# Kernel optimization log

Hardware: AMD Instinct MI355X
Metric: run time of the kernel (lower is better)

The kernel has to match this reference:

```python
import jax, jax.numpy as jnp
import numpy as np
from jax.scipy.special import logsumexp

B, T, S, V = 64, 1024, 512, 1024


def setup_inputs() -> dict:
    key = jax.random.key(0)
    k_obs, k_emis, k_trans, k_prior = jax.random.split(key, 4)
    observations = jax.random.randint(k_obs, (B, T), 0, V, dtype=jnp.int32)
    emission_table = jax.random.normal(k_emis, (V, S), dtype=jnp.float32)
    transitions = jax.random.normal(k_trans, (S, S), dtype=jnp.float32)
    prior = jax.random.normal(k_prior, (S,), dtype=jnp.float32)
    return {
        "observations": observations,
        "emission_table": emission_table,
        "transitions": transitions,
        "prior": prior,
    }


def reference(observations, emission_table, transitions, prior):
    # alpha_0[b, s] = emission_logits(obs_0)[b, s] + prior[s]
    alpha0 = emission_table[observations[:, 0]] + prior  # [B, S]

    def step(alpha, obs_t):
        # new_alpha[b, j] = emis[b, j] + logsumexp_i(alpha[b, i] + trans[i, j])
        e = emission_table[obs_t]  # [B, S]
        a = e + logsumexp(alpha[:, :, None] + transitions[None, :, :], axis=1)
        return a, None

    # scan over time steps 1..T-1; xs is [T-1, B]
    alpha, _ = jax.lax.scan(step, alpha0, observations[:, 1:].T)
    return logsumexp(alpha, axis=1)  # [B]
```

## Files before the change

kernel.cpp:

```cpp
#include <hip/hip_runtime.h>


constexpr int Bn = 64, Tn = 1024, Sn = 512;
#define L2E 1.44269504f

typedef int v4i __attribute__((ext_vector_type(4)));

#if __has_builtin(__builtin_amdgcn_update_dpp)
template <int CTRL>
__device__ __forceinline__ float dpp_fmax(float x) {
    int s = __builtin_bit_cast(int, x);
    int d = __builtin_amdgcn_update_dpp(s, s, CTRL, 0xf, 0xf, false);
    return fmaxf(x, __builtin_bit_cast(float, d));
}
__device__ __forceinline__ float wave_max64(float x) {
    x = dpp_fmax<0x121>(x);
    x = dpp_fmax<0x122>(x);
    x = dpp_fmax<0x124>(x);
    x = dpp_fmax<0x128>(x);
    x = dpp_fmax<0x142>(x);
    x = dpp_fmax<0x143>(x);
    return __builtin_bit_cast(float,
        __builtin_amdgcn_readlane(__builtin_bit_cast(int, x), 63));
}
__device__ __forceinline__ float max_of_8_pattern(float x) {
    x = dpp_fmax<0x121>(x);
    x = dpp_fmax<0x122>(x);
    x = dpp_fmax<0x124>(x);
    return x;
}
#else
__device__ __forceinline__ float wave_max64(float x) {
    #pragma unroll
    for (int off = 32; off; off >>= 1) x = fmaxf(x, __shfl_xor(x, off, 64));
    return x;
}
__device__ __forceinline__ float max_of_8_pattern(float x) {
    #pragma unroll
    for (int off = 1; off < 8; off <<= 1) x = fmaxf(x, __shfl_xor(x, off, 64));
    return x;
}
#endif

__device__ __forceinline__ int bfrag_addr(int i, int c) {
    return ((((c >> 4) * 8 + (i >> 6)) * 64) + ((i >> 4) & 3) * 16 + (c & 15)) * 16
           + (i & 15);
}

__global__ __launch_bounds__(256) void prep_rows(
    const float* __restrict__ trans, unsigned char* __restrict__ EqB,
    float* __restrict__ rowmax)
{
    const int i = blockIdx.x;
    const int j = threadIdx.x;
    const int lane = j & 63, wv = j >> 6;
    float t0 = trans[i * Sn + j];
    float t1 = trans[i * Sn + j + 256];
    float m = fmaxf(t0, t1);
    #pragma unroll
    for (int off = 32; off; off >>= 1) m = fmaxf(m, __shfl_xor(m, off, 64));
    __shared__ float rm[4];
    if (lane == 0) rm[wv] = m;
    __syncthreads();
    m = fmaxf(fmaxf(rm[0], rm[1]), fmaxf(rm[2], rm[3]));
    if (j == 0) rowmax[i] = m;
    int q0 = __float2int_rn(127.f * __expf(t0 - m));
    int q1 = __float2int_rn(127.f * __expf(t1 - m));
    EqB[bfrag_addr(i, j)] = (unsigned char)q0;
    EqB[bfrag_addr(i, j + 256)] = (unsigned char)q1;
}

__global__ __launch_bounds__(512) void prep_scale(
    const float* __restrict__ rowmax, float* __restrict__ lr,
    float* __restrict__ Cp)
{
    const int i = threadIdx.x;
    const int lane = i & 63, wv = i >> 6;
    float m = rowmax[i];
    float rm = m;
    #pragma unroll
    for (int off = 32; off; off >>= 1) rm = fmaxf(rm, __shfl_xor(rm, off, 64));
    __shared__ float red[8];
    if (lane == 0) red[wv] = rm;
    __syncthreads();
    float RM = red[0];
    #pragma unroll
    for (int w = 1; w < 8; ++w) RM = fmaxf(RM, red[w]);
    lr[i] = (m - RM) * L2E + 6.98868469f;
    if (i == 0) *Cp = RM - 9.68837417f;
}

__global__ __launch_bounds__(512, 2) void hmm_fwd(
    const int* __restrict__ obs,
    const float* __restrict__ emis,
    const float* __restrict__ prior,
    const v4i* __restrict__ EqB4,
    const float* __restrict__ lr,
    const float* __restrict__ Cp,
    float* __restrict__ out)
{
    const int b = blockIdx.x;
    const int tid = threadIdx.x;
    const int lane = tid & 63, wv = tid >> 6;
    const int q = lane >> 4;

    __shared__ int obs_s[Tn];
    __shared__ __align__(16) unsigned char Pq[2][Sn];
    __shared__ float redm[2][8];
    __shared__ float reds[8];

    obs_s[tid] = obs[b * Tn + tid];
    obs_s[tid + 512] = obs[b * Tn + 512 + tid];

    v4i Bf[4][8];
    #pragma unroll
    for (int tau = 0; tau < 4; ++tau)
        #pragma unroll
        for (int kap = 0; kap < 8; ++kap)
            Bf[tau][kap] = EqB4[((wv * 4 + tau) * 8 + kap) * 64 + lane];

    const float lr_t = lr[tid];
    const float C = *Cp;

    __syncthreads();

    float a = emis[obs_s[0] * Sn + tid] + prior[tid];
    float e_next = emis[obs_s[1] * Sn + tid];

    for (int t = 1; t < Tn; ++t) {
        const int pb = t & 1;

        float mw = wave_max64(a);
        if (lane == 0) redm[pb][wv] = mw;
        __syncthreads();
        float m = max_of_8_pattern(redm[pb][lane & 7]);

        int gi = __float2int_rn(exp2f(fmaf(a - m, L2E, lr_t)));
        Pq[pb][tid] = (unsigned char)gi;
        __syncthreads();

        float e_cur = e_next;
        if (t < Tn - 1) e_next = emis[obs_s[t + 1] * Sn + tid];

        const unsigned char* Pbase = Pq[pb] + q * 16;
        v4i Af[8];
        #pragma unroll
        for (int kap = 0; kap < 8; ++kap)
            Af[kap] = *(const v4i*)(Pbase + kap * 64);

        v4i acc[4];
        #pragma unroll
        for (int tau = 0; tau < 4; ++tau) {
            v4i z = {0, 0, 0, 0};
            #pragma unroll
            for (int kap = 0; kap < 8; ++kap)
                z = __builtin_amdgcn_mfma_i32_16x16x64_i8(Af[kap], Bf[tau][kap],
                                                          z, 0, 0, 0);
            acc[tau] = z;
        }

        int idot = (lane < 16) ? acc[0].x
                 : (lane < 32) ? acc[1].x
                 : (lane < 48) ? acc[2].x
                               : acc[3].x;

        a = e_cur + m + C + __logf((float)idot);
    }

    float m = a;
    #pragma unroll
    for (int off = 32; off; off >>= 1) m = fmaxf(m, __shfl_xor(m, off, 64));
    if (lane == 0) redm[0][wv] = m;
    __syncthreads();
    #pragma unroll
    for (int w = 0; w < 8; ++w) m = fmaxf(m, redm[0][w]);

    float s = __expf(a - m);
    #pragma unroll
    for (int off = 32; off; off >>= 1) s += __shfl_xor(s, off, 64);
    if (lane == 0) reds[wv] = s;
    __syncthreads();
    if (tid == 0) {
        float tot = 0.f;
        #pragma unroll
        for (int w = 0; w < 8; ++w) tot += reds[w];
        out[b] = m + __logf(tot);
    }
}

extern "C" void kernel_launch(void* const* d_in, const int* in_sizes, int n_in,
                              void* d_out, int out_size, void* d_ws, size_t ws_size,
                              hipStream_t stream) {
    const int*   obs   = (const int*)d_in[0];
    const float* emis  = (const float*)d_in[1];
    const float* trans = (const float*)d_in[2];
    const float* prior = (const float*)d_in[3];
    float* out = (float*)d_out;

    unsigned char* EqB = (unsigned char*)d_ws;
    float* rowmax = (float*)(EqB + Sn * Sn);
    float* lr     = rowmax + Sn;
    float* Cp     = lr + Sn;

    prep_rows<<<Sn, 256, 0, stream>>>(trans, EqB, rowmax);
    prep_scale<<<1, Sn, 0, stream>>>(rowmax, lr, Cp);
    hmm_fwd<<<Bn, Sn, 0, stream>>>(obs, emis, prior,
                                   (const v4i*)EqB, lr, Cp, out);
}
```

Before: 1.010 ms.

## Use per-wave max for quantization to drop one barrier per step

Each wave now quantizes its alpha slice against its own wave-local max, so the block-wide max barrier before writing Pq is removed and only one __syncthreads per time step remains. To compensate, the int8 MFMA reduction is split per K-chunk (per wave). The integer partial sums are then rescaled in float by exp(wave_max - global_max) and combined. This adds eight separate MFMA accumulations per tau instead of chained ones, plus readlane broadcasts and FMAs. It also changes the quantization precision per wave.

```diff
diff --git a/kernel.cpp b/kernel.cpp
--- a/kernel.cpp
+++ b/kernel.cpp
@@ -29,6 +29,10 @@
     x = dpp_fmax<0x124>(x);
     return x;
 }
+__device__ __forceinline__ float lane_bcast(float x, int l) {
+    return __builtin_bit_cast(float,
+        __builtin_amdgcn_readlane(__builtin_bit_cast(int, x), l));
+}
 #else
 __device__ __forceinline__ float wave_max64(float x) {
     #pragma unroll
@@ -39,6 +43,9 @@
     #pragma unroll
     for (int off = 1; off < 8; off <<= 1) x = fmaxf(x, __shfl_xor(x, off, 64));
     return x;
+}
+__device__ __forceinline__ float lane_bcast(float x, int l) {
+    return __shfl(x, l, 64);
 }
 #endif
 
@@ -132,13 +139,14 @@
 
         float mw = wave_max64(a);
         if (lane == 0) redm[pb][wv] = mw;
-        __syncthreads();
-        float m = max_of_8_pattern(redm[pb][lane & 7]);
-
-        int gi = __float2int_rn(exp2f(fmaf(a - m, L2E, lr_t)));
+        int gi = __float2int_rn(exp2f(fmaf(a - mw, L2E, lr_t)));
         Pq[pb][tid] = (unsigned char)gi;
         __syncthreads();
 
+        float r = redm[pb][lane & 7];
+        float m = max_of_8_pattern(r);
+        float sv = exp2f((r - m) * L2E);
+
         float e_cur = e_next;
         if (t < Tn - 1) e_next = emis[obs_s[t + 1] * Sn + tid];
 
@@ -148,23 +156,25 @@
         for (int kap = 0; kap < 8; ++kap)
             Af[kap] = *(const v4i*)(Pbase + kap * 64);
 
-        v4i acc[4];
+        int xw[8];
         #pragma unroll
         for (int tau = 0; tau < 4; ++tau) {
-            v4i z = {0, 0, 0, 0};
+            const v4i z = {0, 0, 0, 0};
             #pragma unroll
-            for (int kap = 0; kap < 8; ++kap)
-                z = __builtin_amdgcn_mfma_i32_16x16x64_i8(Af[kap], Bf[tau][kap],
-                                                          z, 0, 0, 0);
-            acc[tau] = z;
+            for (int w = 0; w < 8; ++w) {
+                v4i acc = __builtin_amdgcn_mfma_i32_16x16x64_i8(
+                    Af[w], Bf[tau][w], z, 0, 0, 0);
+                if (tau == 0) xw[w] = acc.x;
+                else         xw[w] = (q == tau) ? acc.x : xw[w];
+            }
         }
 
-        int idot = (lane < 16) ? acc[0].x
-                 : (lane < 32) ? acc[1].x
-                 : (lane < 48) ? acc[2].x
-                               : acc[3].x;
-
-        a = e_cur + m + C + __logf((float)idot);
+        float fs = 0.f;
+        #pragma unroll
+        for (int w = 0; w < 8; ++w)
+            fs = fmaf(lane_bcast(sv, w), (float)xw[w], fs);
+
+        a = e_cur + m + C + __logf(fs);
     }
 
     float m = a;
```

New measurement: 1.086 ms. 7.5% more time.

## Split transition matvec between MFMA and VALU sdot4 paths

Applied to the files above, without the earlier changes.

Halves the K dimension handled by the int8 MFMA chain. The other half of the 512-state contraction (states 256..511) is now computed on vector ALUs using sdot4 against a register-resident repacked transition slice, 64 ints per thread. The aim is to shorten the serial MFMA dependency chain on each time step by overlapping matrix-core and VALU work. The cost is much higher register pressure (64 extra VGPRs), which may hurt the 2-blocks occupancy target or cause spills, plus an extra packed copy of the transitions in workspace.

```diff
diff --git a/kernel.cpp b/kernel.cpp
--- a/kernel.cpp
+++ b/kernel.cpp
@@ -5,6 +5,18 @@
 #define L2E 1.44269504f
 
 typedef int v4i __attribute__((ext_vector_type(4)));
+
+__device__ __forceinline__ int dot4(int e, int p, int acc) {
+#if __has_builtin(__builtin_amdgcn_sdot4)
+    return __builtin_amdgcn_sdot4(e, p, acc, false);
+#else
+    acc += (int)(signed char)(e) * (int)(signed char)(p);
+    acc += (int)(signed char)(e >> 8) * (int)(signed char)(p >> 8);
+    acc += (int)(signed char)(e >> 16) * (int)(signed char)(p >> 16);
+    acc += (int)(signed char)(e >> 24) * (int)(signed char)(p >> 24);
+    return acc;
+#endif
+}
 
 #if __has_builtin(__builtin_amdgcn_update_dpp)
 template <int CTRL>
@@ -49,7 +61,7 @@
 
 __global__ __launch_bounds__(256) void prep_rows(
     const float* __restrict__ trans, unsigned char* __restrict__ EqB,
-    float* __restrict__ rowmax)
+    unsigned char* __restrict__ E2, float* __restrict__ rowmax)
 {
     const int i = blockIdx.x;
     const int j = threadIdx.x;
@@ -68,6 +80,8 @@
     int q1 = __float2int_rn(127.f * __expf(t1 - m));
     EqB[bfrag_addr(i, j)] = (unsigned char)q0;
     EqB[bfrag_addr(i, j + 256)] = (unsigned char)q1;
+    E2[(i >> 2) * 2048 + j * 4 + (i & 3)] = (unsigned char)q0;
+    E2[(i >> 2) * 2048 + (j + 256) * 4 + (i & 3)] = (unsigned char)q1;
 }
 
 __global__ __launch_bounds__(512) void prep_scale(
@@ -95,6 +109,7 @@
     const float* __restrict__ emis,
     const float* __restrict__ prior,
     const v4i* __restrict__ EqB4,
+    const int* __restrict__ E2u,
     const float* __restrict__ lr,
     const float* __restrict__ Cp,
     float* __restrict__ out)
@@ -112,12 +127,16 @@
     obs_s[tid] = obs[b * Tn + tid];
     obs_s[tid + 512] = obs[b * Tn + 512 + tid];
 
-    v4i Bf[4][8];
+    v4i Bf[4][4];
     #pragma unroll
     for (int tau = 0; tau < 4; ++tau)
         #pragma unroll
-        for (int kap = 0; kap < 8; ++kap)
+        for (int kap = 0; kap < 4; ++kap)
             Bf[tau][kap] = EqB4[((wv * 4 + tau) * 8 + kap) * 64 + lane];
+
+    int Ed[64];
+    #pragma unroll
+    for (int k = 0; k < 64; ++k) Ed[k] = E2u[(64 + k) * Sn + tid];
 
     const float lr_t = lr[tid];
     const float C = *Cp;
@@ -143,9 +162,9 @@
         if (t < Tn - 1) e_next = emis[obs_s[t + 1] * Sn + tid];
 
         const unsigned char* Pbase = Pq[pb] + q * 16;
-        v4i Af[8];
-        #pragma unroll
-        for (int kap = 0; kap < 8; ++kap)
+        v4i Af[4];
+        #pragma unroll
+        for (int kap = 0; kap < 4; ++kap)
             Af[kap] = *(const v4i*)(Pbase + kap * 64);
 
         v4i acc[4];
@@ -153,18 +172,30 @@
         for (int tau = 0; tau < 4; ++tau) {
             v4i z = {0, 0, 0, 0};
             #pragma unroll
-            for (int kap = 0; kap < 8; ++kap)
+            for (int kap = 0; kap < 4; ++kap)
                 z = __builtin_amdgcn_mfma_i32_16x16x64_i8(Af[kap], Bf[tau][kap],
                                                           z, 0, 0, 0);
             acc[tau] = z;
         }
 
-        int idot = (lane < 16) ? acc[0].x
-                 : (lane < 32) ? acc[1].x
-                 : (lane < 48) ? acc[2].x
-                               : acc[3].x;
-
-        a = e_cur + m + C + __logf((float)idot);
+        const v4i* Pd = (const v4i*)(Pq[pb] + 256);
+        int ac0 = 0, ac1 = 0, ac2 = 0, ac3 = 0;
+        #pragma unroll
+        for (int c = 0; c < 16; ++c) {
+            v4i p = Pd[c];
+            ac0 = dot4(Ed[4 * c + 0], p.x, ac0);
+            ac1 = dot4(Ed[4 * c + 1], p.y, ac1);
+            ac2 = dot4(Ed[4 * c + 2], p.z, ac2);
+            ac3 = dot4(Ed[4 * c + 3], p.w, ac3);
+        }
+        int idsum = (ac0 + ac1) + (ac2 + ac3);
+
+        int im = (lane < 16) ? acc[0].x
+               : (lane < 32) ? acc[1].x
+               : (lane < 48) ? acc[2].x
+                             : acc[3].x;
+
+        a = e_cur + m + C + __logf((float)(im + idsum));
     }
 
     float m = a;
@@ -198,12 +229,14 @@
     float* out = (float*)d_out;
 
     unsigned char* EqB = (unsigned char*)d_ws;
-    float* rowmax = (float*)(EqB + Sn * Sn);
+    unsigned char* E2  = EqB + Sn * Sn;
+    float* rowmax = (float*)(E2 + Sn * Sn);
     float* lr     = rowmax + Sn;
     float* Cp     = lr + Sn;
 
-    prep_rows<<<Sn, 256, 0, stream>>>(trans, EqB, rowmax);
+    prep_rows<<<Sn, 256, 0, stream>>>(trans, EqB, E2, rowmax);
     prep_scale<<<1, Sn, 0, stream>>>(rowmax, lr, Cp);
     hmm_fwd<<<Bn, Sn, 0, stream>>>(obs, emis, prior,
-                                   (const v4i*)EqB, lr, Cp, out);
-}
+                                   (const v4i*)EqB, (const int*)E2,
+                                   lr, Cp, out);
+}
```

After: 1.182 ms. 17.0% more time.

## Switch forward recursion matmul to block-scaled FP6 MFMA with per-block exponents

Applied to the files above, without the earlier changes.

Replaces the int8 16x16x64 MFMA path with the gfx950 scaled f8f6f4 16x16x128 MFMA, using FP6 (e2m3) operands and per-32-element E8M0 block scales for both the transition matrix and the per-step probability vector. Halves the MFMA instruction count per step and shrinks the shared-memory probability buffer. It adds in-register 6-bit packing through DPP and shuffles each step, plus readlane scale broadcasts. It also merges the two prep kernels into one. The trade is lower mantissa precision against better dynamic range, and the per-step packing adds latency to a sequential chain.

```diff
diff --git a/kernel.cpp b/kernel.cpp
--- a/kernel.cpp
+++ b/kernel.cpp
@@ -4,13 +4,17 @@
 constexpr int Bn = 64, Tn = 1024, Sn = 512;
 #define L2E 1.44269504f
 
-typedef int v4i __attribute__((ext_vector_type(4)));
-
-#if __has_builtin(__builtin_amdgcn_update_dpp)
+typedef int v8i __attribute__((ext_vector_type(8)));
+typedef float v4f __attribute__((ext_vector_type(4)));
+
+template <int CTRL>
+__device__ __forceinline__ int dpp_i(int x) {
+    return __builtin_amdgcn_update_dpp(x, x, CTRL, 0xf, 0xf, false);
+}
 template <int CTRL>
 __device__ __forceinline__ float dpp_fmax(float x) {
     int s = __builtin_bit_cast(int, x);
-    int d = __builtin_amdgcn_update_dpp(s, s, CTRL, 0xf, 0xf, false);
+    int d = dpp_i<CTRL>(s);
     return fmaxf(x, __builtin_bit_cast(float, d));
 }
 __device__ __forceinline__ float wave_max64(float x) {
@@ -29,98 +33,91 @@
     x = dpp_fmax<0x124>(x);
     return x;
 }
-#else
-__device__ __forceinline__ float wave_max64(float x) {
-    #pragma unroll
-    for (int off = 32; off; off >>= 1) x = fmaxf(x, __shfl_xor(x, off, 64));
-    return x;
-}
-__device__ __forceinline__ float max_of_8_pattern(float x) {
-    #pragma unroll
-    for (int off = 1; off < 8; off <<= 1) x = fmaxf(x, __shfl_xor(x, off, 64));
-    return x;
-}
-#endif
-
-__device__ __forceinline__ int bfrag_addr(int i, int c) {
-    return ((((c >> 4) * 8 + (i >> 6)) * 64) + ((i >> 4) & 3) * 16 + (c & 15)) * 16
-           + (i & 15);
-}
-
-__global__ __launch_bounds__(256) void prep_rows(
-    const float* __restrict__ trans, unsigned char* __restrict__ EqB,
-    float* __restrict__ rowmax)
+__device__ __forceinline__ int rl_i(int x, int l) {
+    return __builtin_amdgcn_readlane(x, l);
+}
+
+__device__ __forceinline__ int e2m3_rn(float v) {
+    v = fminf(v, 7.5f);
+    float mult = v < 2.f ? 8.f : (v < 4.f ? 4.f : 2.f);
+    int   add  = v < 2.f ? 0   : (v < 4.f ? 8   : 16);
+    return (int)rintf(v * mult) + add;
+}
+
+__global__ __launch_bounds__(64) void prep_E6(
+    const float* __restrict__ trans, unsigned int* __restrict__ EqB6,
+    unsigned char* __restrict__ SBtab)
 {
-    const int i = blockIdx.x;
-    const int j = threadIdx.x;
-    const int lane = j & 63, wv = j >> 6;
-    float t0 = trans[i * Sn + j];
-    float t1 = trans[i * Sn + j + 256];
-    float m = fmaxf(t0, t1);
-    #pragma unroll
-    for (int off = 32; off; off >>= 1) m = fmaxf(m, __shfl_xor(m, off, 64));
-    __shared__ float rm[4];
-    if (lane == 0) rm[wv] = m;
-    __syncthreads();
-    m = fmaxf(fmaxf(rm[0], rm[1]), fmaxf(rm[2], rm[3]));
-    if (j == 0) rowmax[i] = m;
-    int q0 = __float2int_rn(127.f * __expf(t0 - m));
-    int q1 = __float2int_rn(127.f * __expf(t1 - m));
-    EqB[bfrag_addr(i, j)] = (unsigned char)q0;
-    EqB[bfrag_addr(i, j + 256)] = (unsigned char)q1;
-}
-
-__global__ __launch_bounds__(512) void prep_scale(
-    const float* __restrict__ rowmax, float* __restrict__ lr,
-    float* __restrict__ Cp)
-{
-    const int i = threadIdx.x;
-    const int lane = i & 63, wv = i >> 6;
-    float m = rowmax[i];
-    float rm = m;
-    #pragma unroll
-    for (int off = 32; off; off >>= 1) rm = fmaxf(rm, __shfl_xor(rm, off, 64));
-    __shared__ float red[8];
-    if (lane == 0) red[wv] = rm;
-    __syncthreads();
-    float RM = red[0];
-    #pragma unroll
-    for (int w = 1; w < 8; ++w) RM = fmaxf(RM, red[w]);
-    lr[i] = (m - RM) * L2E + 6.98868469f;
-    if (i == 0) *Cp = RM - 9.68837417f;
+    const int t = threadIdx.x;
+    const int j = blockIdx.x * 4 + (t >> 4);
+    const int rb = t & 15;
+
+    float tv[32]; float tmax = -1e30f;
+    #pragma unroll
+    for (int k = 0; k < 32; ++k) {
+        tv[k] = trans[(rb * 32 + k) * Sn + j];
+        tmax = fmaxf(tmax, tv[k]);
+    }
+    float e = ceilf(fmaf(tmax, L2E, -2.9068906f));
+
+    unsigned dw[6] = {0, 0, 0, 0, 0, 0};
+    #pragma unroll
+    for (int k = 0; k < 32; ++k) {
+        float v = exp2f(fmaf(tv[k], L2E, -e));
+        unsigned c = (unsigned)e2m3_rn(v);
+        int bit = 6 * k;
+        dw[bit >> 5] |= c << (bit & 31);
+        if ((bit & 31) > 26) dw[(bit >> 5) + 1] |= c >> (32 - (bit & 31));
+    }
+
+    int f = ((j >> 6) * 4 + ((j >> 4) & 3)) * 4 + (rb >> 2);
+    int lane = (rb & 3) * 16 + (j & 15);
+    unsigned base = (unsigned)(f * 64 + lane) * 6;
+    #pragma unroll
+    for (int d = 0; d < 6; ++d) EqB6[base + d] = dw[d];
+
+    int sb = 127 + (int)e;
+    SBtab[j * 16 + rb] = (unsigned char)(sb < 1 ? 1 : (sb > 254 ? 254 : sb));
 }
 
 __global__ __launch_bounds__(512, 2) void hmm_fwd(
     const int* __restrict__ obs,
     const float* __restrict__ emis,
     const float* __restrict__ prior,
-    const v4i* __restrict__ EqB4,
-    const float* __restrict__ lr,
-    const float* __restrict__ Cp,
+    const unsigned int* __restrict__ EqB6,
+    const unsigned char* __restrict__ SBtab,
     float* __restrict__ out)
 {
     const int b = blockIdx.x;
     const int tid = threadIdx.x;
     const int lane = tid & 63, wv = tid >> 6;
     const int q = lane >> 4;
+    const int hb = lane >> 5;
 
     __shared__ int obs_s[Tn];
-    __shared__ __align__(16) unsigned char Pq[2][Sn];
+    __shared__ __align__(16) unsigned int Pq6[2][96];
     __shared__ float redm[2][8];
     __shared__ float reds[8];
 
     obs_s[tid] = obs[b * Tn + tid];
     obs_s[tid + 512] = obs[b * Tn + 512 + tid];
 
-    v4i Bf[4][8];
-    #pragma unroll
-    for (int tau = 0; tau < 4; ++tau)
-        #pragma unroll
-        for (int kap = 0; kap < 8; ++kap)
-            Bf[tau][kap] = EqB4[((wv * 4 + tau) * 8 + kap) * 64 + lane];
-
-    const float lr_t = lr[tid];
-    const float C = *Cp;
+    v8i Bf8[4][4];
+    int SBv[4][4];
+    #pragma unroll
+    for (int tau = 0; tau < 4; ++tau) {
+        int col = wv * 64 + tau * 16 + (lane & 15);
+        #pragma unroll
+        for (int kap = 0; kap < 4; ++kap) {
+            const uint2* p = (const uint2*)(EqB6 +
+                (unsigned)((((wv * 4 + tau) * 4 + kap) * 64 + lane) * 6));
+            uint2 x0 = p[0], x1 = p[1], x2 = p[2];
+            v8i bb = {(int)x0.x, (int)x0.y, (int)x1.x, (int)x1.y,
+                      (int)x2.x, (int)x2.y, 0, 0};
+            Bf8[tau][kap] = bb;
+            SBv[tau][kap] = (int)SBtab[col * 16 + kap * 4 + q] * 0x01010101;
+        }
+    }
 
     __syncthreads();
 
@@ -133,38 +130,77 @@
         float mw = wave_max64(a);
         if (lane == 0) redm[pb][wv] = mw;
         __syncthreads();
-        float m = max_of_8_pattern(redm[pb][lane & 7]);
-
-        int gi = __float2int_rn(exp2f(fmaf(a - m, L2E, lr_t)));
-        Pq[pb][tid] = (unsigned char)gi;
+
+        float r = redm[pb][lane & 7];
+        float mAll = max_of_8_pattern(r);
+
+        float nf = fmaxf(floorf((r - mAll) * L2E), -110.f);
+        int sb = 126 + (int)nf;
+        int sbdup = sb * 0x01010101;
+
+        float nown = fmaxf(floorf((mw - mAll) * L2E), -110.f);
+
+        float v = exp2f(fmaf(a - mAll, L2E, 1.0f - nown));
+        int code = e2m3_rn(v);
+
+        int p1 = dpp_i<0xB1>(code);
+        int m1 = (lane & 1) ? (p1 | (code << 6)) : (code | (p1 << 6));
+        int p2 = dpp_i<0x4E>(m1);
+        int w24 = (lane & 2) ? (p2 | (m1 << 12)) : (m1 | (p2 << 12));
+
+        int rowbase = lane & 48;
+        int w1 = __shfl(w24, rowbase + 4, 64);
+        int w2 = __shfl(w24, rowbase + 8, 64);
+        int w3 = __shfl(w24, rowbase + 12, 64);
+        int sel = lane & 15;
+        unsigned dwv = sel == 0 ? (unsigned)(w24 | (w1 << 24))
+                     : sel == 1 ? (unsigned)(((unsigned)w1 >> 8) | (w2 << 16))
+                                : (unsigned)(((unsigned)w2 >> 16) | (w3 << 8));
+        if (sel < 3) Pq6[pb][3 * (tid >> 4) + sel] = dwv;
+
+        int ee0 = rl_i(sbdup, 0), ee1 = rl_i(sbdup, 1);
+        int ee2 = rl_i(sbdup, 2), ee3 = rl_i(sbdup, 3);
+        int ee4 = rl_i(sbdup, 4), ee5 = rl_i(sbdup, 5);
+        int ee6 = rl_i(sbdup, 6), ee7 = rl_i(sbdup, 7);
+        int sA0 = hb ? ee1 : ee0;
+        int sA1 = hb ? ee3 : ee2;
+        int sA2 = hb ? ee5 : ee4;
+        int sA3 = hb ? ee7 : ee6;
         __syncthreads();
 
         float e_cur = e_next;
         if (t < Tn - 1) e_next = emis[obs_s[t + 1] * Sn + tid];
 
-        const unsigned char* Pbase = Pq[pb] + q * 16;
-        v4i Af[8];
-        #pragma unroll
-        for (int kap = 0; kap < 8; ++kap)
-            Af[kap] = *(const v4i*)(Pbase + kap * 64);
-
-        v4i acc[4];
+        v8i Af8[4];
+        #pragma unroll
+        for (int kap = 0; kap < 4; ++kap) {
+            const uint2* pp = (const uint2*)(Pq6[pb] + kap * 24 + q * 6);
+            uint2 x0 = pp[0], x1 = pp[1], x2 = pp[2];
+            v8i aa = {(int)x0.x, (int)x0.y, (int)x1.x, (int)x1.y,
+                      (int)x2.x, (int)x2.y, 0, 0};
+            Af8[kap] = aa;
+        }
+
+        float accx[4];
         #pragma unroll
         for (int tau = 0; tau < 4; ++tau) {
-            v4i z = {0, 0, 0, 0};
+            v4f z = {0.f, 0.f, 0.f, 0.f};
             #pragma unroll
-            for (int kap = 0; kap < 8; ++kap)
-                z = __builtin_amdgcn_mfma_i32_16x16x64_i8(Af[kap], Bf[tau][kap],
-                                                          z, 0, 0, 0);
-            acc[tau] = z;
+            for (int kap = 0; kap < 4; ++kap) {
+                int sA = (kap == 0) ? sA0 : (kap == 1) ? sA1
+                         : (kap == 2) ? sA2 : sA3;
+                z = __builtin_amdgcn_mfma_scale_f32_16x16x128_f8f6f4(
+                        Af8[kap], Bf8[tau][kap], z, 2, 2, 0, sA, 0, SBv[tau][kap]);
+            }
+            accx[tau] = z.x;
         }
 
-        int idot = (lane < 16) ? acc[0].x
-                 : (lane < 32) ? acc[1].x
-                 : (lane < 48) ? acc[2].x
-                               : acc[3].x;
-
-        a = e_cur + m + C + __logf((float)idot);
+        float fs = (lane < 16) ? accx[0]
+                 : (lane < 32) ? accx[1]
+                 : (lane < 48) ? accx[2]
+                               : accx[3];
+
+        a = e_cur + mAll + __logf(fs);
     }
 
     float m = a;
@@ -197,13 +233,9 @@
     const float* prior = (const float*)d_in[3];
     float* out = (float*)d_out;
 
-    unsigned char* EqB = (unsigned char*)d_ws;
-    float* rowmax = (float*)(EqB + Sn * Sn);
-    float* lr     = rowmax + Sn;
-    float* Cp     = lr + Sn;
-
-    prep_rows<<<Sn, 256, 0, stream>>>(trans, EqB, rowmax);
-    prep_scale<<<1, Sn, 0, stream>>>(rowmax, lr, Cp);
-    hmm_fwd<<<Bn, Sn, 0, stream>>>(obs, emis, prior,
-                                   (const v4i*)EqB, lr, Cp, out);
-}
+    unsigned int* EqB6 = (unsigned int*)d_ws;
+    unsigned char* SBtab = (unsigned char*)d_ws + Sn * Sn * 6 / 8;
+
+    prep_E6<<<Sn / 4, 64, 0, stream>>>(trans, EqB6, SBtab);
+    hmm_fwd<<<Bn, Sn, 0, stream>>>(obs, emis, prior, EqB6, SBtab, out);
+}
```

Result: slower. 1.143 ms (+13.2%).
